# Optimization experiments

Hardware: AMD Instinct MI355X
Metric: run time of the kernel (lower is better)

## Reference

```python
import jax, jax.numpy as jnp
import numpy as np

B, C, N = 8, 3, 4096
NSAMPLE = 10
MLP = (64, 64)
# checkerboard re-gather pattern from the original module
INDS = np.array([0, 1, 2, 3, 2, 3, 4, 5, 4, 5, 6, 7, 6, 7, 8, 9])


def setup_inputs() -> dict:
    key = jax.random.key(0)
    k1, k2, k3 = jax.random.split(key, 3)
    pos = jax.random.normal(k1, (B, C, N), jnp.float32)
    w1 = jax.random.normal(k2, (MLP[0], 4 * C, 2, 2), jnp.float32) * 0.1  # Conv2d(12, mlp0, k=2)
    b1 = jnp.zeros((MLP[0],), jnp.float32)
    w2 = jax.random.normal(k3, (MLP[1], MLP[0]), jnp.float32) * 0.1       # Conv2d(mlp0, mlp1, k=1)
    b2 = jnp.zeros((MLP[1],), jnp.float32)
    return {"pos": pos, "w1": w1, "b1": b1, "w2": w2, "b2": b2}


def _squeeze_2x2_alt(x):
    # x: [B, N, c, 4, 4] -> [B, N, 4c, 2, 2] with channel order [a, d, b, c]
    a = x[..., 0::2, 0::2]  # (0,0) of each 2x2 block
    d = x[..., 1::2, 1::2]  # (1,1)
    b = x[..., 0::2, 1::2]  # (0,1)
    c = x[..., 1::2, 0::2]  # (1,0)
    return jnp.concatenate([a, d, b, c], axis=-3)


def reference(pos, w1, b1, w2, b2):
    Bn, Cn, Nn = pos.shape
    pos_t = pos.transpose(0, 2, 1)  # [B, N, C]
    # pairwise squared distances [B, N, N]
    sq = jnp.sum(pos_t * pos_t, axis=-1)
    d2 = sq[:, :, None] - 2.0 * jnp.einsum('bnc,bmc->bnm', pos_t, pos_t) + sq[:, None, :]
    _, idx = jax.lax.top_k(-d2, NSAMPLE)  # [B, N, K] nearest neighbors (self first)
    # grouping_operation: grouped[b,c,n,k] = pos[b,c,idx[b,n,k]]
    grouped = jax.vmap(lambda p, i: p[:, i])(pos, idx)  # [B, C, N, K]
    pg = grouped[..., INDS]                              # [B, C, N, 16]
    pg = pg.transpose(0, 2, 1, 3).reshape(Bn, Nn, Cn, 4, 4)  # [B, N, 3, 4, 4]
    sqz = _squeeze_2x2_alt(pg)                           # [B, N, 12, 2, 2]
    # Conv2d(12->mlp0, k=2, stride=1) over 2x2 spatial == full contraction
    h = jnp.einsum('bnchw,ochw->bno', sqz, w1) + b1      # [B, N, mlp0]
    out = jnp.einsum('bno,po->bnp', h, w2) + b2          # [B, N, mlp1]
    return out.transpose(0, 2, 1)                        # [B, mlp1, N]
```

## Files before the change

kernel.cpp:

```cpp
#include <hip/hip_runtime.h>
#include <math.h>

#define NPTS 4096
#define NSMP 10

typedef float f32x2 __attribute__((ext_vector_type(2)));
typedef _Float16 half8 __attribute__((ext_vector_type(8)));
typedef float f32x16 __attribute__((ext_vector_type(16)));

__global__ __launch_bounds__(256) void prep_kernel(
    const float* __restrict__ w1, const float* __restrict__ b1,
    const float* __restrict__ w2, const float* __restrict__ b2,
    float* __restrict__ wn, float* __restrict__ bb) {
  __shared__ float w1l[64 * 48];
  __shared__ float w2t[64 * 64];
  __shared__ float b1l[64];
  __shared__ float part[4][30][64];
  __shared__ float bpart[4][64];
  const int t = threadIdx.x, p = t & 63, grp = t >> 6, o0 = grp * 16;
  for (int idx = t; idx < 64 * 48; idx += 256) w1l[idx] = w1[idx];
  for (int idx = t; idx < 64 * 64; idx += 256) w2t[(idx & 63) * 64 + (idx >> 6)] = w2[idx];
  if (t < 64) b1l[t] = b1[t];
  __syncthreads();

  const int sg[16] = {0,2,4,6, 3,5,7,9, 1,3,5,7, 2,4,6,8};
  float w2r[16];
  #pragma unroll
  for (int oo = 0; oo < 16; ++oo) w2r[oo] = w2t[(o0 + oo) * 64 + p];
  float wloc[30];
  #pragma unroll
  for (int i = 0; i < 30; ++i) wloc[i] = 0.0f;
  #pragma unroll
  for (int g = 0; g < 4; ++g)
    #pragma unroll
    for (int i = 0; i < 2; ++i)
      #pragma unroll
      for (int j = 0; j < 2; ++j) {
        const int s = sg[g * 4 + i * 2 + j];
        #pragma unroll
        for (int c = 0; c < 3; ++c) {
          const int k = (c + 3 * g) * 4 + i * 2 + j;
          float wk = 0.0f;
          #pragma unroll
          for (int oo = 0; oo < 16; ++oo)
            wk = fmaf(w2r[oo], w1l[(o0 + oo) * 48 + k], wk);
          wloc[s * 3 + c] += wk;
        }
      }
  #pragma unroll
  for (int i = 0; i < 30; ++i) part[grp][i][p] = wloc[i];
  float sb = 0.0f;
  #pragma unroll
  for (int oo = 0; oo < 16; ++oo) sb = fmaf(w2r[oo], b1l[o0 + oo], sb);
  bpart[grp][p] = sb;
  __syncthreads();
  const float* p0 = &part[0][0][0];
  for (int idx = t; idx < 30 * 64; idx += 256)
    wn[idx] = p0[idx] + p0[1920 + idx] + p0[3840 + idx] + p0[5760 + idx];
  if (t < 64) bb[t] = b2[t] + bpart[0][t] + bpart[1][t] + bpart[2][t] + bpart[3][t];
}

__global__ __launch_bounds__(1024, 4) void topk_kernel(const float* __restrict__ pos,
                                                       const float* __restrict__ wng,
                                                       const float* __restrict__ bbg,
                                                       float* __restrict__ out) {
  __shared__ half8 pts8[NPTS];
  __shared__ float X[16 * 260];
  __shared__ half8 a8[128];
  __shared__ float wl[30 * 64];
  __shared__ float bl[64];
  __shared__ float taub[64];
  __shared__ float slackb[64];
  __shared__ int   cnt[64];
  __shared__ int   nbrT[64][NSMP];

  const int b = blockIdx.y, tid = threadIdx.x, lane = tid & 63, wv = tid >> 6;
  const float* pb = pos + (size_t)b * 3 * NPTS;
  const int nb = blockIdx.x * 64;

  for (int i = tid; i < NPTS; i += 1024) {
    float x = pb[i], y = pb[i + NPTS], z = pb[i + 2 * NPTS];
    float sq = fmaf(z, z, fmaf(y, y, x * x));
    _Float16 hx = (_Float16)x, hy = (_Float16)y, hz = (_Float16)z, hs = (_Float16)sq;
    _Float16 lx = (_Float16)(x - (float)hx);
    _Float16 ly = (_Float16)(y - (float)hy);
    _Float16 lz = (_Float16)(z - (float)hz);
    _Float16 ls = (_Float16)(sq - (float)hs);
    half8 v = {hx, lx, hy, ly, hz, lz, hs, ls};
    pts8[i] = v;
  }
  if (tid < 64) {
    float qx = pb[nb + tid], qy = pb[nb + tid + NPTS], qz = pb[nb + tid + 2 * NPTS];
    _Float16 ax = (_Float16)(-2.0f * (float)(_Float16)qx);
    _Float16 ay = (_Float16)(-2.0f * (float)(_Float16)qy);
    _Float16 az = (_Float16)(-2.0f * (float)(_Float16)qz);
    _Float16 one = (_Float16)1.0f;
    half8 va = {ax, ax, ay, ay, az, az, one, one};
    half8 vz;
    #pragma unroll
    for (int j = 0; j < 8; ++j) vz[j] = (_Float16)0.0f;
    a8[2 * tid] = va;
    a8[2 * tid + 1] = vz;
    slackb[tid] = 1.5e-3f + 0.012f * (fabsf(qx) + fabsf(qy) + fabsf(qz));
    cnt[tid] = 0;
    bl[tid] = bbg[tid];
  }
  for (int i = tid; i < 30 * 64; i += 1024) wl[i] = wng[i];
  __syncthreads();

  const int qt = wv >> 3, ws = wv & 7, h = lane >> 5, c31 = lane & 31;
  const int base = ws * 512;
  const half8 af = a8[(qt * 32 + c31) * 2 + h];
  f32x16 zz;
  #pragma unroll
  for (int j = 0; j < 16; ++j) zz[j] = 0.0f;

  float mreg[16];
  #pragma unroll
  for (int j = 0; j < 16; ++j) mreg[j] = INFINITY;
  #pragma unroll
  for (int t = 0; t < 16; ++t) {
    half8 bf = pts8[base + t * 32 + c31];
    f32x16 acc = __builtin_amdgcn_mfma_f32_32x32x16_f16(af, bf, zz, 0, 0, 0);
    #pragma unroll
    for (int j = 0; j < 16; ++j) mreg[j] = fminf(mreg[j], acc[j]);
  }
  #pragma unroll
  for (int j = 0; j < 16; ++j) {
    mreg[j] = fminf(mreg[j], __shfl_xor(mreg[j], 1));
    mreg[j] = fminf(mreg[j], __shfl_xor(mreg[j], 2));
  }
  if ((lane & 3) == 0) {
    const int g = (lane >> 2) & 7;
    #pragma unroll
    for (int j = 0; j < 16; ++j) {
      const int row = qt * 32 + (j & 3) + 8 * (j >> 2) + 4 * h;
      X[row * 64 + ws * 8 + g] = mreg[j];
    }
  }
  __syncthreads();

  unsigned um[4];
  #pragma unroll
  for (int r = 0; r < 4; ++r) {
    float dm = X[(4 * wv + r) * 64 + lane];
    unsigned ub = __float_as_uint(dm);
    um[r] = (ub & 0x80000000u) ? ~ub : (ub | 0x80000000u);
  }
  unsigned pfx0 = 0u, pfx1 = 0u, pfx2 = 0u, pfx3 = 0u;
  #pragma unroll 1
  for (int bno = 31; bno >= 8; --bno) {
    const unsigned bit = 1u << bno, ones = bit - 1u;
    if (__popcll(__ballot(um[0] <= (pfx0 | ones))) < NSMP) pfx0 |= bit;
    if (__popcll(__ballot(um[1] <= (pfx1 | ones))) < NSMP) pfx1 |= bit;
    if (__popcll(__ballot(um[2] <= (pfx2 | ones))) < NSMP) pfx2 |= bit;
    if (__popcll(__ballot(um[3] <= (pfx3 | ones))) < NSMP) pfx3 |= bit;
  }
  float tx[4];
  #pragma unroll
  for (int r = 0; r < 4; ++r) {
    unsigned T = ((r == 0) ? pfx0 : (r == 1) ? pfx1 : (r == 2) ? pfx2 : pfx3) | 0xFFu;
    unsigned tb = (T & 0x80000000u) ? (T ^ 0x80000000u) : ~T;
    float tf = __uint_as_float(tb);
    tx[r] = __fadd_rn(__fadd_rn(tf, slackb[4 * wv + r]), __fmul_rn(fabsf(tf), 1e-5f));
  }
  if (lane == 0) {
    taub[4 * wv + 0] = tx[0]; taub[4 * wv + 1] = tx[1];
    taub[4 * wv + 2] = tx[2]; taub[4 * wv + 3] = tx[3];
  }
  __syncthreads();

  float tau16[16];
  #pragma unroll
  for (int j = 0; j < 16; ++j) tau16[j] = taub[qt * 32 + (j & 3) + 8 * (j >> 2) + 4 * h];
  int* bufi = (int*)X;
  #pragma unroll 2
  for (int t = 0; t < 16; ++t) {
    const int m0 = base + t * 32 + c31;
    half8 bf = pts8[m0];
    f32x16 acc = __builtin_amdgcn_mfma_f32_32x32x16_f16(af, bf, zz, 0, 0, 0);
    #pragma unroll
    for (int j = 0; j < 16; ++j) {
      if (acc[j] <= tau16[j]) {
        const int row = qt * 32 + (j & 3) + 8 * (j >> 2) + 4 * h;
        int ps = atomicAdd(&cnt[row], 1);
        if (ps < 64) bufi[row * 64 + ps] = m0;
      }
    }
  }
  __syncthreads();

  int c[4], si[4], rank[4];
  double dd[4];
  int cmax = 0;
  #pragma unroll
  for (int r = 0; r < 4; ++r) {
    c[r] = __builtin_amdgcn_readfirstlane(cnt[4 * wv + r]);
    if (c[r] > 64) c[r] = 64;
    cmax = (c[r] > cmax) ? c[r] : cmax;
    rank[r] = 0;
  }
  #pragma unroll
  for (int r = 0; r < 4; ++r) {
    const int nq = nb + 4 * wv + r;
    float qxf = pb[nq], qyf = pb[nq + NPTS], qzf = pb[nq + 2 * NPTS];
    if (lane < c[r]) {
      si[r] = bufi[(4 * wv + r) * 64 + lane];
      float px = pb[si[r]], py = pb[si[r] + NPTS], pz = pb[si[r] + 2 * NPTS];
      double dqx = (double)qxf, dqy = (double)qyf, dqz = (double)qzf;
      double dpx = (double)px, dpy = (double)py, dpz = (double)pz;
      double dot = dqx * dpx + dqy * dpy + dqz * dpz;
      double sqn = dqx * dqx + dqy * dqy + dqz * dqz;
      double sqm = dpx * dpx + dpy * dpy + dpz * dpz;
      dd[r] = (sqn - 2.0 * dot) + sqm;
    } else { dd[r] = (double)INFINITY; si[r] = 0x7FFFFFFF; }
  }
  #pragma unroll 1
  for (int j = 0; j < cmax; ++j) {
    #pragma unroll
    for (int r = 0; r < 4; ++r) {
      int jlo = __builtin_amdgcn_readlane(__double2loint(dd[r]), j);
      int jhi = __builtin_amdgcn_readlane(__double2hiint(dd[r]), j);
      int ji  = __builtin_amdgcn_readlane(si[r], j);
      double jd = __hiloint2double(jhi, jlo);
      if (jd < dd[r] || (jd == dd[r] && ji < si[r])) ++rank[r];
    }
  }
  #pragma unroll
  for (int r = 0; r < 4; ++r)
    if (lane < c[r] && rank[r] < NSMP)
      nbrT[4 * wv + r][rank[r]] = si[r];
  __syncthreads();

  float* transF = &X[wv * 260];
  #pragma unroll 1
  for (int r = 0; r < 4; ++r) {
    float a = bl[lane];
    #pragma unroll
    for (int s = 0; s < NSMP; ++s) {
      const int id = nbrT[4 * wv + r][s];
      float px = pb[id], py = pb[id + NPTS], pz = pb[id + 2 * NPTS];
      a = fmaf(wl[(s * 3 + 0) * 64 + lane], px, a);
      a = fmaf(wl[(s * 3 + 1) * 64 + lane], py, a);
      a = fmaf(wl[(s * 3 + 2) * 64 + lane], pz, a);
    }
    transF[r * 65 + lane] = a;
  }
  __syncthreads();

  {
    int p = tid >> 4, t16 = tid & 15;
    float4 v;
    v.x = X[t16 * 260 + 0 * 65 + p];
    v.y = X[t16 * 260 + 1 * 65 + p];
    v.z = X[t16 * 260 + 2 * 65 + p];
    v.w = X[t16 * 260 + 3 * 65 + p];
    *(float4*)(out + ((size_t)b * 64 + p) * NPTS + nb + 4 * t16) = v;
  }
}

extern "C" void kernel_launch(void* const* d_in, const int* in_sizes, int n_in,
                              void* d_out, int out_size, void* d_ws, size_t ws_size,
                              hipStream_t stream) {
  (void)in_sizes; (void)n_in; (void)out_size; (void)ws_size;
  const float* pos = (const float*)d_in[0];
  const float* w1  = (const float*)d_in[1];
  const float* b1  = (const float*)d_in[2];
  const float* w2  = (const float*)d_in[3];
  const float* b2  = (const float*)d_in[4];
  float* out = (float*)d_out;

  float* wn = (float*)d_ws;
  float* bb = (float*)((char*)d_ws + 30 * 64 * 4);

  prep_kernel<<<dim3(1), dim3(256), 0, stream>>>(w1, b1, w2, b2, wn, bb);
  topk_kernel<<<dim3(64, 8), dim3(1024), 0, stream>>>(pos, wn, bb, out);
}
```

Baseline: 141.1 us.

## Drop hi/lo fp16 split in distance MFMA, widen slack with geometric bound

The candidate-distance MFMA now uses plain fp16 coordinates (half4 per point) instead of hi/lo split half8, halving the LDS footprint of the point table. The coarse threshold slack is recomputed from a geometric error bound based on the query norm and kth-distance, to cover the larger fp16 rounding error. Launch bounds are raised to 8 waves-per-EU hints and loops are left un-unrolled to cut register use. The trade-off is more candidates passing the looser threshold, and the risk that the slack fails to cover fp16 error for some inputs.

```diff
diff --git a/kernel.cpp b/kernel.cpp
--- a/kernel.cpp
+++ b/kernel.cpp
@@ -4,7 +4,7 @@
 #define NPTS 4096
 #define NSMP 10
 
-typedef float f32x2 __attribute__((ext_vector_type(2)));
+typedef _Float16 half4 __attribute__((ext_vector_type(4)));
 typedef _Float16 half8 __attribute__((ext_vector_type(8)));
 typedef float f32x16 __attribute__((ext_vector_type(16)));
 
@@ -60,17 +60,17 @@
   if (t < 64) bb[t] = b2[t] + bpart[0][t] + bpart[1][t] + bpart[2][t] + bpart[3][t];
 }
 
-__global__ __launch_bounds__(1024, 4) void topk_kernel(const float* __restrict__ pos,
+__global__ __launch_bounds__(1024, 8) void topk_kernel(const float* __restrict__ pos,
                                                        const float* __restrict__ wng,
                                                        const float* __restrict__ bbg,
                                                        float* __restrict__ out) {
-  __shared__ half8 pts8[NPTS];
+  __shared__ half4 pts4[NPTS];
   __shared__ float X[16 * 260];
-  __shared__ half8 a8[128];
+  __shared__ half4 a4s[64];
   __shared__ float wl[30 * 64];
   __shared__ float bl[64];
   __shared__ float taub[64];
-  __shared__ float slackb[64];
+  __shared__ float sqqs[64];
   __shared__ int   cnt[64];
   __shared__ int   nbrT[64][NSMP];
 
@@ -81,27 +81,17 @@
   for (int i = tid; i < NPTS; i += 1024) {
     float x = pb[i], y = pb[i + NPTS], z = pb[i + 2 * NPTS];
     float sq = fmaf(z, z, fmaf(y, y, x * x));
-    _Float16 hx = (_Float16)x, hy = (_Float16)y, hz = (_Float16)z, hs = (_Float16)sq;
-    _Float16 lx = (_Float16)(x - (float)hx);
-    _Float16 ly = (_Float16)(y - (float)hy);
-    _Float16 lz = (_Float16)(z - (float)hz);
-    _Float16 ls = (_Float16)(sq - (float)hs);
-    half8 v = {hx, lx, hy, ly, hz, lz, hs, ls};
-    pts8[i] = v;
+    half4 v = {(_Float16)x, (_Float16)y, (_Float16)z, (_Float16)sq};
+    pts4[i] = v;
   }
   if (tid < 64) {
     float qx = pb[nb + tid], qy = pb[nb + tid + NPTS], qz = pb[nb + tid + 2 * NPTS];
-    _Float16 ax = (_Float16)(-2.0f * (float)(_Float16)qx);
-    _Float16 ay = (_Float16)(-2.0f * (float)(_Float16)qy);
-    _Float16 az = (_Float16)(-2.0f * (float)(_Float16)qz);
-    _Float16 one = (_Float16)1.0f;
-    half8 va = {ax, ax, ay, ay, az, az, one, one};
-    half8 vz;
-    #pragma unroll
-    for (int j = 0; j < 8; ++j) vz[j] = (_Float16)0.0f;
-    a8[2 * tid] = va;
-    a8[2 * tid + 1] = vz;
-    slackb[tid] = 1.5e-3f + 0.012f * (fabsf(qx) + fabsf(qy) + fabsf(qz));
+    half4 va = {(_Float16)(-2.0f * (float)(_Float16)qx),
+                (_Float16)(-2.0f * (float)(_Float16)qy),
+                (_Float16)(-2.0f * (float)(_Float16)qz),
+                (_Float16)1.0f};
+    a4s[tid] = va;
+    sqqs[tid] = fmaf(qz, qz, fmaf(qy, qy, qx * qx));
     cnt[tid] = 0;
     bl[tid] = bbg[tid];
   }
@@ -110,7 +100,13 @@
 
   const int qt = wv >> 3, ws = wv & 7, h = lane >> 5, c31 = lane & 31;
   const int base = ws * 512;
-  const half8 af = a8[(qt * 32 + c31) * 2 + h];
+  half8 af;
+  #pragma unroll
+  for (int j = 0; j < 8; ++j) af[j] = (_Float16)0.0f;
+  {
+    half4 aq = a4s[qt * 32 + c31];
+    if (h == 0) { af[0] = aq[0]; af[1] = aq[1]; af[2] = aq[2]; af[3] = aq[3]; }
+  }
   f32x16 zz;
   #pragma unroll
   for (int j = 0; j < 16; ++j) zz[j] = 0.0f;
@@ -118,9 +114,13 @@
   float mreg[16];
   #pragma unroll
   for (int j = 0; j < 16; ++j) mreg[j] = INFINITY;
-  #pragma unroll
+  #pragma unroll 1
   for (int t = 0; t < 16; ++t) {
-    half8 bf = pts8[base + t * 32 + c31];
+    half4 bp = pts4[base + t * 32 + c31];
+    half8 bf;
+    #pragma unroll
+    for (int j = 0; j < 8; ++j) bf[j] = (_Float16)0.0f;
+    bf[0] = bp[0]; bf[1] = bp[1]; bf[2] = bp[2]; bf[3] = bp[3];
     f32x16 acc = __builtin_amdgcn_mfma_f32_32x32x16_f16(af, bf, zz, 0, 0, 0);
     #pragma unroll
     for (int j = 0; j < 16; ++j) mreg[j] = fminf(mreg[j], acc[j]);
@@ -162,7 +162,13 @@
     unsigned T = ((r == 0) ? pfx0 : (r == 1) ? pfx1 : (r == 2) ? pfx2 : pfx3) | 0xFFu;
     unsigned tb = (T & 0x80000000u) ? (T ^ 0x80000000u) : ~T;
     float tf = __uint_as_float(tb);
-    tx[r] = __fadd_rn(__fadd_rn(tf, slackb[4 * wv + r]), __fmul_rn(fabsf(tf), 1e-5f));
+    float sqr = sqqs[4 * wv + r];
+    float d10sq = tf + sqr;
+    if (d10sq < 0.0f) d10sq = 0.0f;
+    float aq = sqrtf(sqr);
+    float L = aq + sqrtf(d10sq) + 0.05f;
+    float slack = 2e-3f + 0.00146484375f * (4.0f * aq * L + L * L);
+    tx[r] = __fadd_rn(tf, slack);
   }
   if (lane == 0) {
     taub[4 * wv + 0] = tx[0]; taub[4 * wv + 1] = tx[1];
@@ -174,10 +180,14 @@
   #pragma unroll
   for (int j = 0; j < 16; ++j) tau16[j] = taub[qt * 32 + (j & 3) + 8 * (j >> 2) + 4 * h];
   int* bufi = (int*)X;
-  #pragma unroll 2
+  #pragma unroll 1
   for (int t = 0; t < 16; ++t) {
     const int m0 = base + t * 32 + c31;
-    half8 bf = pts8[m0];
+    half4 bp = pts4[m0];
+    half8 bf;
+    #pragma unroll
+    for (int j = 0; j < 8; ++j) bf[j] = (_Float16)0.0f;
+    bf[0] = bp[0]; bf[1] = bp[1]; bf[2] = bp[2]; bf[3] = bp[3];
     f32x16 acc = __builtin_amdgcn_mfma_f32_32x32x16_f16(af, bf, zz, 0, 0, 0);
     #pragma unroll
     for (int j = 0; j < 16; ++j) {
```

Result: slower. 153.3 us (+8.7%).
